# Kernel optimization log

Hardware: AMD Instinct MI355X
Metric: run time of the kernel (lower is better)

Reference implementation:

```python
import jax, jax.numpy as jnp
from jax import lax
import numpy as np

B, T, H, E = 4096, 16, 1024, 1024


def setup_inputs() -> dict:
    key = jax.random.key(0)
    ks = jax.random.split(key, 6)
    query = jax.random.normal(ks[0], (B, H), dtype=jnp.float32)
    topics = jax.random.normal(ks[1], (B, T, E), dtype=jnp.float32)
    coverage_vector = jax.random.uniform(ks[2], (B, T), dtype=jnp.float32)
    # Ua: Linear(embed->hidden, bias=False); weight [H, E]
    Ua_w = jax.random.normal(ks[3], (H, E), dtype=jnp.float32) * 0.03
    # Wa: Linear(hidden->hidden, bias=False). Applied repeatedly (T times) to
    # query in the original loop, so keep spectral norm < 1 for stability.
    Wa_w = jax.random.normal(ks[4], (H, H), dtype=jnp.float32) * 0.01
    # va: Linear(hidden->1, bias=True)
    va_w = jax.random.normal(ks[5], (1, H), dtype=jnp.float32) * 0.03
    va_b = jnp.zeros((1,), dtype=jnp.float32)
    return {"query": query, "topics": topics, "coverage_vector": coverage_vector,
            "Ua_w": Ua_w, "Wa_w": Wa_w, "va_w": va_w, "va_b": va_b}


def reference(query, topics, coverage_vector, Ua_w, Wa_w, va_w, va_b):
    # proj_key for all steps at once: Ua(topics[:, i, :]) -> [B, T, H]
    proj_keys = jnp.einsum('bte,he->bth', topics, Ua_w)
    # Original loop mutates query = Wa(query) each step, so step i uses
    # Wa^(i+1) @ query. Sequential dependence -> lax.scan over T.
    def step(q, pk_c):
        pk, c = pk_c                       # pk: [B, H], c: [B]
        q = q @ Wa_w.T                     # query = Wa(query)
        s = (jnp.tanh(q + pk) @ va_w.T)[:, 0] + va_b[0]  # va(tanh(.)) -> [B]
        return q, s * c                    # scale by coverage C_t[:, i]
    xs = (jnp.swapaxes(proj_keys, 0, 1), coverage_vector.T)  # [T,B,H], [T,B]
    _, scores = lax.scan(step, query, xs)  # scores: [T, B]
    scores = scores.T                      # [B, T]
    alphas = jax.nn.softmax(scores, axis=1)
    mt = jnp.einsum('bt,bte->be', alphas, topics)  # bmm(alphas[:,None,:], topics)
    return mt, alphas
```

## Files before the change

kernel.cpp:

```cpp
#include <hip/hip_runtime.h>

typedef unsigned short u16;
typedef unsigned int u32;
typedef __attribute__((ext_vector_type(8))) __bf16 bf16x8;
typedef __attribute__((ext_vector_type(4))) float f32x4;

__device__ __forceinline__ u16 f2bf(float f) {
  u32 u = __float_as_uint(f);
  u32 r = (u + 0x7FFFu + ((u >> 16) & 1u)) >> 16;
  return (u16)r;
}

__device__ __forceinline__ void gload_lds16(const void* g, void* l) {
  __builtin_amdgcn_global_load_lds((const __attribute__((address_space(1))) u32*)g,
                                   (__attribute__((address_space(3))) u32*)l, 16, 0, 0);
}

__device__ __forceinline__ float fast_tanh(float x) {
  x = fminf(fmaxf(x, -15.f), 15.f);
  float e2 = __expf(2.f * x);
  return (e2 - 1.f) / (e2 + 1.f);
}

__global__ __launch_bounds__(256) void cvt_kernel(const float* __restrict__ src,
                                                  u16* __restrict__ dst, int n4) {
  int i = blockIdx.x * blockDim.x + threadIdx.x;
  if (i >= n4) return;
  float4 v = reinterpret_cast<const float4*>(src)[i];
  ushort4 o;
  o.x = f2bf(v.x); o.y = f2bf(v.y); o.z = f2bf(v.z); o.w = f2bf(v.w);
  reinterpret_cast<ushort4*>(dst)[i] = o;
}

__global__ __launch_bounds__(256) void cvt3_kernel(const float* __restrict__ q_src, u16* __restrict__ q_dst,
                                                   const float* __restrict__ u_src, u16* __restrict__ u_dst,
                                                   const float* __restrict__ w_src, u16* __restrict__ w_dst) {
  int b = blockIdx.x;
  const float* src; u16* dst; int i;
  if (b < 4096)      { src = q_src; dst = q_dst; i = b * 256 + threadIdx.x; }
  else if (b < 5120) { src = u_src; dst = u_dst; i = (b - 4096) * 256 + threadIdx.x; }
  else               { src = w_src; dst = w_dst; i = (b - 5120) * 256 + threadIdx.x; }
  float4 v = reinterpret_cast<const float4*>(src)[i];
  ushort4 o;
  o.x = f2bf(v.x); o.y = f2bf(v.y); o.z = f2bf(v.z); o.w = f2bf(v.w);
  reinterpret_cast<ushort4*>(dst)[i] = o;
}

__global__ __launch_bounds__(256) void transpose_bf16_kernel(const float* __restrict__ src,
                                                             u16* __restrict__ dst) {
  __shared__ float tile[32][33];
  int tx = threadIdx.x & 31, ty = threadIdx.x >> 5;
  int bx = blockIdx.x * 32, by = blockIdx.y * 32;
#pragma unroll
  for (int j = 0; j < 32; j += 8)
    tile[ty + j][tx] = src[(size_t)(by + ty + j) * 1024 + bx + tx];
  __syncthreads();
#pragma unroll
  for (int j = 0; j < 32; j += 8)
    dst[(size_t)(bx + ty + j) * 1024 + by + tx] = f2bf(tile[tx][ty + j]);
}

__device__ __forceinline__ void stage_tile(const u16* __restrict__ g, size_t row_stride,
                                           u16* lds, int tid) {
#pragma unroll
  for (int s = 0; s < 4; ++s) {
    int chunk = s * 256 + tid;
    const u16* gp = g + (size_t)(chunk >> 3) * row_stride + (size_t)((chunk & 7) * 8);
    u16* lp = lds + (tid >> 6) * 512 + s * 2048;
    gload_lds16(gp, lp);
  }
}

struct PowArgs {
  const u16* A[8];
  const u16* Bt[8];
  u16* C[8];
  u16* Ct[8];
};

__global__ __launch_bounds__(256) void pow_gemm_kernel(PowArgs args) {
  const u16* A  = args.A[blockIdx.z];
  const u16* Bt = args.Bt[blockIdx.z];
  u16* C  = args.C[blockIdx.z];
  u16* Ct = args.Ct[blockIdx.z];

  __shared__ __align__(16) u16 As[8192];
  __shared__ __align__(16) u16 Bs[8192];

  int tid = threadIdx.x;
  int lane = tid & 63, wave = tid >> 6;
  int wr = wave >> 1, wc = wave & 1;
  int lr = lane & 15, lg = lane >> 4;
  int m0 = blockIdx.x * 128, n0 = blockIdx.y * 128;

  f32x4 acc[4][4];
  const f32x4 zero = {0.f, 0.f, 0.f, 0.f};
#pragma unroll
  for (int m = 0; m < 4; ++m)
#pragma unroll
    for (int n = 0; n < 4; ++n) acc[m][n] = zero;

  for (int k0 = 0; k0 < 1024; k0 += 64) {
    stage_tile(A + (size_t)m0 * 1024 + k0, 1024, As, tid);
    stage_tile(Bt + (size_t)n0 * 1024 + k0, 1024, Bs, tid);
    __syncthreads();
#pragma unroll
    for (int ks = 0; ks < 2; ++ks) {
      bf16x8 a[4], b[4];
#pragma unroll
      for (int m = 0; m < 4; ++m)
        a[m] = *reinterpret_cast<const bf16x8*>(As + (wr * 64 + m * 16 + lr) * 64 + ks * 32 + lg * 8);
#pragma unroll
      for (int n = 0; n < 4; ++n)
        b[n] = *reinterpret_cast<const bf16x8*>(Bs + (wc * 64 + n * 16 + lr) * 64 + ks * 32 + lg * 8);
#pragma unroll
      for (int m = 0; m < 4; ++m)
#pragma unroll
        for (int n = 0; n < 4; ++n)
          acc[m][n] = __builtin_amdgcn_mfma_f32_16x16x32_bf16(a[m], b[n], acc[m][n], 0, 0, 0);
    }
    __syncthreads();
  }

#pragma unroll
  for (int m = 0; m < 4; ++m) {
    int row0 = m0 + wr * 64 + m * 16 + lg * 4;
#pragma unroll
    for (int n = 0; n < 4; ++n) {
      int col = n0 + wc * 64 + n * 16 + lr;
      f32x4 c = acc[m][n];
      ushort4 pk;
      pk.x = f2bf(c[0]); pk.y = f2bf(c[1]); pk.z = f2bf(c[2]); pk.w = f2bf(c[3]);
      C[(size_t)(row0 + 0) * 1024 + col] = pk.x;
      C[(size_t)(row0 + 1) * 1024 + col] = pk.y;
      C[(size_t)(row0 + 2) * 1024 + col] = pk.z;
      C[(size_t)(row0 + 3) * 1024 + col] = pk.w;
      *reinterpret_cast<ushort4*>(Ct + (size_t)col * 1024 + row0) = pk;
    }
  }
}

__global__ __launch_bounds__(256) void score_gemm_kernel(
    const u16* __restrict__ query_bf, const u16* __restrict__ topics_bf,
    const u16* __restrict__ F_base, const u16* __restrict__ Ua_bf,
    const float* __restrict__ va_w, float* __restrict__ scores_raw) {
  __shared__ __align__(16) u16 As[8192];
  __shared__ __align__(16) u16 Bs[8192];
  __shared__ float sbuf[128];

  int tid = threadIdx.x;
  int lane = tid & 63, wave = tid >> 6;
  int wr = wave >> 1, wc = wave & 1;
  int lr = lane & 15, lg = lane >> 4;
  int m0 = blockIdx.x * 128, n0 = blockIdx.y * 128;
  int t = blockIdx.z;

  if (tid < 128) sbuf[tid] = 0.f;

  const u16* Ft = F_base + (size_t)t * (1024 * 1024);

  f32x4 acc[4][4];
  const f32x4 zero = {0.f, 0.f, 0.f, 0.f};
#pragma unroll
  for (int m = 0; m < 4; ++m)
#pragma unroll
    for (int n = 0; n < 4; ++n) acc[m][n] = zero;

  for (int k0 = 0; k0 < 2048; k0 += 64) {
    const u16* asrc; size_t astr;
    const u16* bsrc;
    if (k0 < 1024) {
      asrc = query_bf + (size_t)m0 * 1024 + k0; astr = 1024;
      bsrc = Ft + (size_t)n0 * 1024 + k0;
    } else {
      asrc = topics_bf + (size_t)m0 * 16384 + (size_t)t * 1024 + (size_t)(k0 - 1024); astr = 16384;
      bsrc = Ua_bf + (size_t)n0 * 1024 + (size_t)(k0 - 1024);
    }
    stage_tile(asrc, astr, As, tid);
    stage_tile(bsrc, 1024, Bs, tid);
    __syncthreads();
#pragma unroll
    for (int ks = 0; ks < 2; ++ks) {
      bf16x8 a[4], b[4];
#pragma unroll
      for (int m = 0; m < 4; ++m)
        a[m] = *reinterpret_cast<const bf16x8*>(As + (wr * 64 + m * 16 + lr) * 64 + ks * 32 + lg * 8);
#pragma unroll
      for (int n = 0; n < 4; ++n)
        b[n] = *reinterpret_cast<const bf16x8*>(Bs + (wc * 64 + n * 16 + lr) * 64 + ks * 32 + lg * 8);
#pragma unroll
      for (int m = 0; m < 4; ++m)
#pragma unroll
        for (int n = 0; n < 4; ++n)
          acc[m][n] = __builtin_amdgcn_mfma_f32_16x16x32_bf16(a[m], b[n], acc[m][n], 0, 0, 0);
    }
    __syncthreads();
  }

  float va_c[4];
#pragma unroll
  for (int n = 0; n < 4; ++n) va_c[n] = va_w[n0 + wc * 64 + n * 16 + lr];

#pragma unroll
  for (int m = 0; m < 4; ++m) {
    float rs[4] = {0.f, 0.f, 0.f, 0.f};
#pragma unroll
    for (int n = 0; n < 4; ++n) {
      f32x4 c = acc[m][n];
      rs[0] += va_c[n] * fast_tanh(c[0]);
      rs[1] += va_c[n] * fast_tanh(c[1]);
      rs[2] += va_c[n] * fast_tanh(c[2]);
      rs[3] += va_c[n] * fast_tanh(c[3]);
    }
#pragma unroll
    for (int j = 0; j < 4; ++j) {
      float v = rs[j];
      v += __shfl_xor(v, 1);
      v += __shfl_xor(v, 2);
      v += __shfl_xor(v, 4);
      v += __shfl_xor(v, 8);
      if (lr == 0) atomicAdd(&sbuf[wr * 64 + m * 16 + lg * 4 + j], v);
    }
  }
  __syncthreads();
  if (tid < 128) atomicAdd(&scores_raw[(size_t)(m0 + tid) * 16 + t], sbuf[tid]);
}

__global__ __launch_bounds__(256) void softmax_mt_kernel(
    const float* __restrict__ scores_raw, const float* __restrict__ cov,
    const float* __restrict__ topics, const float* __restrict__ va_b,
    float* __restrict__ mt, float* __restrict__ alphas) {
  int b = blockIdx.x;
  int tid = threadIdx.x;
  float vb = va_b[0];
  float e[16];
  float mx = -3.4e38f;
#pragma unroll
  for (int t = 0; t < 16; ++t) {
    float s = (scores_raw[b * 16 + t] + vb) * cov[b * 16 + t];
    e[t] = s;
    mx = fmaxf(mx, s);
  }
  float sum = 0.f;
#pragma unroll
  for (int t = 0; t < 16; ++t) { e[t] = __expf(e[t] - mx); sum += e[t]; }
  float inv = 1.f / sum;
  if (tid == 0) {
#pragma unroll
    for (int t = 0; t < 16; ++t) alphas[b * 16 + t] = e[t] * inv;
  }
  const float4* tp = reinterpret_cast<const float4*>(topics + (size_t)b * 16384);
  float4 accv = {0.f, 0.f, 0.f, 0.f};
#pragma unroll
  for (int t = 0; t < 16; ++t) {
    float4 v = tp[t * 256 + tid];
    float a = e[t] * inv;
    accv.x += a * v.x; accv.y += a * v.y; accv.z += a * v.z; accv.w += a * v.w;
  }
  reinterpret_cast<float4*>(mt + (size_t)b * 1024)[tid] = accv;
}

extern "C" void kernel_launch(void* const* d_in, const int* in_sizes, int n_in,
                              void* d_out, int out_size, void* d_ws, size_t ws_size,
                              hipStream_t stream) {
  (void)in_sizes; (void)n_in; (void)out_size; (void)ws_size;
  const float* query = (const float*)d_in[0];
  const float* topics = (const float*)d_in[1];
  const float* cov   = (const float*)d_in[2];
  const float* Ua    = (const float*)d_in[3];
  const float* Wa    = (const float*)d_in[4];
  const float* va_w  = (const float*)d_in[5];
  const float* va_b  = (const float*)d_in[6];

  float* mt = (float*)d_out;
  float* alphas = mt + (size_t)4096 * 1024;

  char* ws = (char*)d_ws;
  u16* topics_bf = (u16*)(ws);
  u16* query_bf  = (u16*)(ws + (size_t)128 * 1024 * 1024);
  u16* Ua_bf     = (u16*)(ws + (size_t)136 * 1024 * 1024);
  u16* F_base    = (u16*)(ws + (size_t)138 * 1024 * 1024);
  u16* FT_base   = (u16*)(ws + (size_t)170 * 1024 * 1024);
  float* scores_raw = (float*)(ws + (size_t)202 * 1024 * 1024);

  hipMemsetAsync(scores_raw, 0, (size_t)4096 * 16 * sizeof(float), stream);

  cvt_kernel<<<65536, 256, 0, stream>>>(topics, topics_bf, 16777216);
  cvt3_kernel<<<6144, 256, 0, stream>>>(query, query_bf, Ua, Ua_bf, Wa, F_base);
  transpose_bf16_kernel<<<dim3(32, 32), 256, 0, stream>>>(Wa, FT_base);

  const size_t MS = 1024 * 1024;
  auto F  = [&](int i) { return F_base + (size_t)i * MS; };
  auto FT = [&](int i) { return FT_base + (size_t)i * MS; };

  PowArgs a1{};
  a1.A[0] = F(0); a1.Bt[0] = FT(0); a1.C[0] = F(1); a1.Ct[0] = FT(1);
  pow_gemm_kernel<<<dim3(8, 8, 1), 256, 0, stream>>>(a1);
  PowArgs a2{};
  a2.A[0] = F(1); a2.Bt[0] = FT(0); a2.C[0] = F(2); a2.Ct[0] = FT(2);
  a2.A[1] = F(1); a2.Bt[1] = FT(1); a2.C[1] = F(3); a2.Ct[1] = FT(3);
  pow_gemm_kernel<<<dim3(8, 8, 2), 256, 0, stream>>>(a2);
  PowArgs a3{};
  for (int p = 0; p < 4; ++p) { a3.A[p] = F(3); a3.Bt[p] = FT(p); a3.C[p] = F(4 + p); a3.Ct[p] = FT(4 + p); }
  pow_gemm_kernel<<<dim3(8, 8, 4), 256, 0, stream>>>(a3);
  PowArgs a4{};
  for (int p = 0; p < 8; ++p) { a4.A[p] = F(7); a4.Bt[p] = FT(p); a4.C[p] = F(8 + p); a4.Ct[p] = FT(8 + p); }
  pow_gemm_kernel<<<dim3(8, 8, 8), 256, 0, stream>>>(a4);

  score_gemm_kernel<<<dim3(32, 8, 16), 256, 0, stream>>>(query_bf, topics_bf, F_base, Ua_bf,
                                                         va_w, scores_raw);
  softmax_mt_kernel<<<4096, 256, 0, stream>>>(scores_raw, cov, topics, va_b, mt, alphas);
}
```

Baseline: 912.0 us.

## Replace score GEMM with 256x256 double-buffered pipelined kernel and swizzled LDS

Replaces the 128x128 score GEMM with a 512-thread, 256x256-tile kernel. It double-buffers 128KB of dynamic LDS, splits each K-step into four phases that interleave async global-to-LDS loads with MFMA bursts, and raises wave priority during the MFMAs. It also XOR-swizzles LDS layouts in both the pow and score GEMMs to reduce bank conflicts. The topics conversion kernel becomes grid-stride with fewer blocks, and the per-block reduction drops LDS atomics for plain stores. The aim is to hide memory latency and raise MFMA utilisation in the dominant GEMM, at the cost of a grid of only 1024 blocks and heavy register and LDS pressure.

```diff
diff --git a/kernel.cpp b/kernel.cpp
--- a/kernel.cpp
+++ b/kernel.cpp
@@ -24,12 +24,13 @@
 
 __global__ __launch_bounds__(256) void cvt_kernel(const float* __restrict__ src,
                                                   u16* __restrict__ dst, int n4) {
-  int i = blockIdx.x * blockDim.x + threadIdx.x;
-  if (i >= n4) return;
-  float4 v = reinterpret_cast<const float4*>(src)[i];
-  ushort4 o;
-  o.x = f2bf(v.x); o.y = f2bf(v.y); o.z = f2bf(v.z); o.w = f2bf(v.w);
-  reinterpret_cast<ushort4*>(dst)[i] = o;
+  int stride = gridDim.x * blockDim.x;
+  for (int i = blockIdx.x * blockDim.x + threadIdx.x; i < n4; i += stride) {
+    float4 v = reinterpret_cast<const float4*>(src)[i];
+    ushort4 o;
+    o.x = f2bf(v.x); o.y = f2bf(v.y); o.z = f2bf(v.z); o.w = f2bf(v.w);
+    reinterpret_cast<ushort4*>(dst)[i] = o;
+  }
 }
 
 __global__ __launch_bounds__(256) void cvt3_kernel(const float* __restrict__ q_src, u16* __restrict__ q_dst,
@@ -65,7 +66,9 @@
 #pragma unroll
   for (int s = 0; s < 4; ++s) {
     int chunk = s * 256 + tid;
-    const u16* gp = g + (size_t)(chunk >> 3) * row_stride + (size_t)((chunk & 7) * 8);
+    int row = chunk >> 3;
+    int kcl = (chunk & 7) ^ (row & 7);
+    const u16* gp = g + (size_t)row * row_stride + (size_t)(kcl * 8);
     u16* lp = lds + (tid >> 6) * 512 + s * 2048;
     gload_lds16(gp, lp);
   }
@@ -108,11 +111,15 @@
     for (int ks = 0; ks < 2; ++ks) {
       bf16x8 a[4], b[4];
 #pragma unroll
-      for (int m = 0; m < 4; ++m)
-        a[m] = *reinterpret_cast<const bf16x8*>(As + (wr * 64 + m * 16 + lr) * 64 + ks * 32 + lg * 8);
-#pragma unroll
-      for (int n = 0; n < 4; ++n)
-        b[n] = *reinterpret_cast<const bf16x8*>(Bs + (wc * 64 + n * 16 + lr) * 64 + ks * 32 + lg * 8);
+      for (int m = 0; m < 4; ++m) {
+        int ra = wr * 64 + m * 16 + lr;
+        a[m] = *reinterpret_cast<const bf16x8*>(As + ra * 64 + (((ks * 4 + lg) ^ (ra & 7)) << 3));
+      }
+#pragma unroll
+      for (int n = 0; n < 4; ++n) {
+        int rb = wc * 64 + n * 16 + lr;
+        b[n] = *reinterpret_cast<const bf16x8*>(Bs + rb * 64 + (((ks * 4 + lg) ^ (rb & 7)) << 3));
+      }
 #pragma unroll
       for (int m = 0; m < 4; ++m)
 #pragma unroll
@@ -140,69 +147,120 @@
   }
 }
 
-__global__ __launch_bounds__(256) void score_gemm_kernel(
+
+#define PHASE_READS(CUR, KS, MH)                                                 \
+  { _Pragma("unroll") for (int i_ = 0; i_ < 4; ++i_) af[i_] = lda(CUR, KS, (MH)*4 + i_); \
+    if ((MH) == 0) { _Pragma("unroll") for (int n_ = 0; n_ < 4; ++n_) bfr[n_] = ldb(CUR, KS, n_); } }
+
+#define PHASE_MFMA(MH)                                                           \
+  { __builtin_amdgcn_s_barrier();                                                \
+    asm volatile("s_waitcnt lgkmcnt(0)" ::: "memory");                           \
+    __builtin_amdgcn_sched_barrier(0);                                           \
+    __builtin_amdgcn_s_setprio(1);                                               \
+    _Pragma("unroll") for (int i_ = 0; i_ < 4; ++i_)                             \
+      _Pragma("unroll") for (int n_ = 0; n_ < 4; ++n_)                           \
+        acc[(MH)*4 + i_][n_] =                                                   \
+            __builtin_amdgcn_mfma_f32_16x16x32_bf16(af[i_], bfr[n_], acc[(MH)*4 + i_][n_], 0, 0, 0); \
+    __builtin_amdgcn_s_setprio(0); }
+
+#define PHASE_END()                                                              \
+  { __builtin_amdgcn_s_barrier(); __builtin_amdgcn_sched_barrier(0); }
+
+__global__ __launch_bounds__(512, 2) void score8_kernel(
     const u16* __restrict__ query_bf, const u16* __restrict__ topics_bf,
     const u16* __restrict__ F_base, const u16* __restrict__ Ua_bf,
     const float* __restrict__ va_w, float* __restrict__ scores_raw) {
-  __shared__ __align__(16) u16 As[8192];
-  __shared__ __align__(16) u16 Bs[8192];
-  __shared__ float sbuf[128];
-
-  int tid = threadIdx.x;
-  int lane = tid & 63, wave = tid >> 6;
-  int wr = wave >> 1, wc = wave & 1;
-  int lr = lane & 15, lg = lane >> 4;
-  int m0 = blockIdx.x * 128, n0 = blockIdx.y * 128;
-  int t = blockIdx.z;
-
-  if (tid < 128) sbuf[tid] = 0.f;
+  extern __shared__ __align__(16) char lds[];
+
+  const int tid = threadIdx.x;
+  const int lane = tid & 63, wave = tid >> 6;
+  const int wm = wave >> 2, wn = wave & 3;
+  const int lr = lane & 15, lg = lane >> 4;
+  const int m0 = blockIdx.x * 256, n0 = blockIdx.y * 256;
+  const int t = blockIdx.z;
+  const int NT = 32;
 
   const u16* Ft = F_base + (size_t)t * (1024 * 1024);
 
-  f32x4 acc[4][4];
+  auto a_src = [&](int kt, const u16*& p, int& str) {
+    if (kt < 16) { p = query_bf + (size_t)m0 * 1024 + kt * 64; str = 1024; }
+    else { p = topics_bf + (size_t)m0 * 16384 + (size_t)t * 1024 + (kt - 16) * 64; str = 16384; }
+  };
+  auto b_src = [&](int kt, const u16*& p, int& str) {
+    if (kt < 16) { p = Ft + (size_t)n0 * 1024 + kt * 64; str = 1024; }
+    else { p = Ua_bf + (size_t)n0 * 1024 + (kt - 16) * 64; str = 1024; }
+  };
+
+  auto stage = [&](const u16* p, int str, int ks, int lds_byte) {
+#pragma unroll
+    for (int s = 0; s < 2; ++s) {
+      int c = s * 512 + tid;
+      int row = c >> 2;
+      int cl = (c & 3) ^ ((row >> 1) & 3);
+      const u16* gp = p + (size_t)row * str + ks * 32 + cl * 8;
+      char* lp = lds + lds_byte + s * 8192 + (tid >> 6) * 1024;
+      gload_lds16(gp, lp);
+    }
+  };
+
+  auto lda = [&](int cur, int ks, int m) -> bf16x8 {
+    int row = wm * 128 + m * 16 + lr;
+    int byte = cur * 65536 + ks * 16384 + row * 64 + ((lg ^ ((row >> 1) & 3)) << 4);
+    return *reinterpret_cast<const bf16x8*>(lds + byte);
+  };
+  auto ldb = [&](int cur, int ks, int n) -> bf16x8 {
+    int row = wn * 64 + n * 16 + lr;
+    int byte = cur * 65536 + 32768 + ks * 16384 + row * 64 + ((lg ^ ((row >> 1) & 3)) << 4);
+    return *reinterpret_cast<const bf16x8*>(lds + byte);
+  };
+
+  f32x4 acc[8][4];
   const f32x4 zero = {0.f, 0.f, 0.f, 0.f};
 #pragma unroll
-  for (int m = 0; m < 4; ++m)
+  for (int m = 0; m < 8; ++m)
 #pragma unroll
     for (int n = 0; n < 4; ++n) acc[m][n] = zero;
 
-  for (int k0 = 0; k0 < 2048; k0 += 64) {
-    const u16* asrc; size_t astr;
-    const u16* bsrc;
-    if (k0 < 1024) {
-      asrc = query_bf + (size_t)m0 * 1024 + k0; astr = 1024;
-      bsrc = Ft + (size_t)n0 * 1024 + k0;
-    } else {
-      asrc = topics_bf + (size_t)m0 * 16384 + (size_t)t * 1024 + (size_t)(k0 - 1024); astr = 16384;
-      bsrc = Ua_bf + (size_t)n0 * 1024 + (size_t)(k0 - 1024);
-    }
-    stage_tile(asrc, astr, As, tid);
-    stage_tile(bsrc, 1024, Bs, tid);
-    __syncthreads();
-#pragma unroll
-    for (int ks = 0; ks < 2; ++ks) {
-      bf16x8 a[4], b[4];
-#pragma unroll
-      for (int m = 0; m < 4; ++m)
-        a[m] = *reinterpret_cast<const bf16x8*>(As + (wr * 64 + m * 16 + lr) * 64 + ks * 32 + lg * 8);
-#pragma unroll
-      for (int n = 0; n < 4; ++n)
-        b[n] = *reinterpret_cast<const bf16x8*>(Bs + (wc * 64 + n * 16 + lr) * 64 + ks * 32 + lg * 8);
-#pragma unroll
-      for (int m = 0; m < 4; ++m)
-#pragma unroll
-        for (int n = 0; n < 4; ++n)
-          acc[m][n] = __builtin_amdgcn_mfma_f32_16x16x32_bf16(a[m], b[n], acc[m][n], 0, 0, 0);
-    }
-    __syncthreads();
+  bf16x8 af[4], bfr[4];
+  const u16 *ap, *bp; int as_, bs_;
+
+  a_src(0, ap, as_); stage(ap, as_, 0, 0);
+  b_src(0, bp, bs_); stage(bp, bs_, 0, 32768);
+  a_src(0, ap, as_); stage(ap, as_, 1, 16384);
+  b_src(0, bp, bs_); stage(bp, bs_, 1, 49152);
+  a_src(1, ap, as_); stage(ap, as_, 0, 65536);
+  b_src(1, bp, bs_); stage(bp, bs_, 0, 65536 + 32768);
+  asm volatile("s_waitcnt vmcnt(4)" ::: "memory");
+  __builtin_amdgcn_s_barrier();
+  __builtin_amdgcn_sched_barrier(0);
+
+#pragma unroll 2
+  for (int kt = 0; kt < NT; ++kt) {
+    int cur = kt & 1, nxt = cur ^ 1;
+    PHASE_READS(cur, 0, 0);
+    if (kt + 1 < NT) { a_src(kt + 1, ap, as_); stage(ap, as_, 1, nxt * 65536 + 16384); }
+    PHASE_MFMA(0); PHASE_END();
+    PHASE_READS(cur, 0, 1);
+    if (kt + 1 < NT) { b_src(kt + 1, bp, bs_); stage(bp, bs_, 1, nxt * 65536 + 49152); }
+    PHASE_MFMA(1); PHASE_END();
+    PHASE_READS(cur, 1, 0);
+    if (kt + 2 < NT) { a_src(kt + 2, ap, as_); stage(ap, as_, 0, cur * 65536); }
+    PHASE_MFMA(0); PHASE_END();
+    PHASE_READS(cur, 1, 1);
+    if (kt + 2 < NT) { b_src(kt + 2, bp, bs_); stage(bp, bs_, 0, cur * 65536 + 32768); }
+    PHASE_MFMA(1);
+    if (kt < NT - 2)       { asm volatile("s_waitcnt vmcnt(4)" ::: "memory"); }
+    else if (kt == NT - 2) { asm volatile("s_waitcnt vmcnt(0)" ::: "memory"); }
+    PHASE_END();
   }
 
   float va_c[4];
 #pragma unroll
-  for (int n = 0; n < 4; ++n) va_c[n] = va_w[n0 + wc * 64 + n * 16 + lr];
-
-#pragma unroll
-  for (int m = 0; m < 4; ++m) {
+  for (int n = 0; n < 4; ++n) va_c[n] = va_w[n0 + wn * 64 + n * 16 + lr];
+
+  float* sred = (float*)lds;
+#pragma unroll
+  for (int m = 0; m < 8; ++m) {
     float rs[4] = {0.f, 0.f, 0.f, 0.f};
 #pragma unroll
     for (int n = 0; n < 4; ++n) {
@@ -219,11 +277,14 @@
       v += __shfl_xor(v, 2);
       v += __shfl_xor(v, 4);
       v += __shfl_xor(v, 8);
-      if (lr == 0) atomicAdd(&sbuf[wr * 64 + m * 16 + lg * 4 + j], v);
+      if (lr == 0) sred[wn * 256 + wm * 128 + m * 16 + lg * 4 + j] = v;
     }
   }
   __syncthreads();
-  if (tid < 128) atomicAdd(&scores_raw[(size_t)(m0 + tid) * 16 + t], sbuf[tid]);
+  if (tid < 256) {
+    float s = sred[tid] + sred[256 + tid] + sred[512 + tid] + sred[768 + tid];
+    atomicAdd(&scores_raw[(size_t)(m0 + tid) * 16 + t], s);
+  }
 }
 
 __global__ __launch_bounds__(256) void softmax_mt_kernel(
@@ -283,9 +344,12 @@
   u16* FT_base   = (u16*)(ws + (size_t)170 * 1024 * 1024);
   float* scores_raw = (float*)(ws + (size_t)202 * 1024 * 1024);
 
+  hipFuncSetAttribute(reinterpret_cast<const void*>(score8_kernel),
+                      hipFuncAttributeMaxDynamicSharedMemorySize, 131072);
+
   hipMemsetAsync(scores_raw, 0, (size_t)4096 * 16 * sizeof(float), stream);
 
-  cvt_kernel<<<65536, 256, 0, stream>>>(topics, topics_bf, 16777216);
+  cvt_kernel<<<8192, 256, 0, stream>>>(topics, topics_bf, 16777216);
   cvt3_kernel<<<6144, 256, 0, stream>>>(query, query_bf, Ua, Ua_bf, Wa, F_base);
   transpose_bf16_kernel<<<dim3(32, 32), 256, 0, stream>>>(Wa, FT_base);
 
@@ -307,7 +371,7 @@
   for (int p = 0; p < 8; ++p) { a4.A[p] = F(7); a4.Bt[p] = FT(p); a4.C[p] = F(8 + p); a4.Ct[p] = FT(8 + p); }
   pow_gemm_kernel<<<dim3(8, 8, 8), 256, 0, stream>>>(a4);
 
-  score_gemm_kernel<<<dim3(32, 8, 16), 256, 0, stream>>>(query_bf, topics_bf, F_base, Ua_bf,
-                                                         va_w, scores_raw);
+  score8_kernel<<<dim3(16, 4, 16), 512, 131072, stream>>>(query_bf, topics_bf, F_base, Ua_bf,
+                                                          va_w, scores_raw);
   softmax_mt_kernel<<<4096, 256, 0, stream>>>(scores_raw, cov, topics, va_b, mt, alphas);
 }
```

Result: faster. 823.0 us (-9.8%).
